# Performance work log

Hardware: AMD Instinct MI355X
Metric: run time of the kernel (lower is better)

## Reference

```python
import jax, jax.numpy as jnp
import numpy as np

N, E, H = 20000, 320000, 5
IND, OUT = 64, 64
D2 = 2 * OUT          # 128
CAT = OUT + D2        # 192
BN_EPS = 1e-5


def _bn(x, g, b, m, v):
    # eval-mode BatchNorm1d
    return (x - m) * jax.lax.rsqrt(v + BN_EPS) * g + b


def _gcn(x, W, b, src, dst, n):
    # PyG GCNConv: add self-loops (already in src/dst), sym-normalized aggregation
    h = x @ W                                             # [N, C]
    deg = jax.ops.segment_sum(jnp.ones_like(dst, dtype=h.dtype), dst, num_segments=n)
    dinv = jnp.where(deg > 0, jax.lax.rsqrt(deg), 0.0)
    norm = dinv[src] * dinv[dst]                          # [E']
    out = jax.ops.segment_sum(h[src] * norm[:, None], dst, num_segments=n)
    return out + b


def _gat(x, W, att_src, att_dst, b, src, dst, n, heads, c):
    # PyG GATConv (concat=False): per-edge attention, segment softmax over dst
    hx = (x @ W).reshape(n, heads, c)                     # [N, H, C]
    a_s = jnp.einsum('nhc,hc->nh', hx, att_src)           # [N, H]
    a_d = jnp.einsum('nhc,hc->nh', hx, att_dst)
    e = jax.nn.leaky_relu(a_s[src] + a_d[dst], 0.2)       # [E', H]
    m = jax.ops.segment_max(e, dst, num_segments=n)       # every node has a self-loop
    w = jnp.exp(e - m[dst])
    den = jax.ops.segment_sum(w, dst, num_segments=n)
    alpha = w / den[dst]                                  # [E', H]
    out = jax.ops.segment_sum(hx[src] * alpha[:, :, None], dst, num_segments=n)  # [N,H,C]
    return out.mean(axis=1) + b


def setup_inputs() -> dict:
    key = jax.random.key(0)
    ks = iter(jax.random.split(key, 64))
    rn = lambda *s: jax.random.normal(next(ks), s, dtype=jnp.float32) * 0.05
    d = {}
    d['x_in'] = jax.random.normal(next(ks), (N, IND), dtype=jnp.float32)
    d['edge_index'] = jax.random.randint(next(ks), (2, E), 0, N, dtype=jnp.int64)
    # nn1: indim -> 2*indim -> outdim -> 2*outdim
    d['nn1_w1'], d['nn1_b1'] = rn(IND, 2 * IND), rn(2 * IND)
    d['nn1_w2'], d['nn1_b2'] = rn(2 * IND, OUT), rn(OUT)
    d['nn1_w3'], d['nn1_b3'] = rn(OUT, D2), rn(D2)
    # batchnorms (eval mode: gamma, beta, running mean/var)
    for name, dim in (('bn0', D2), ('bn1', D2), ('bn2', OUT)):
        d[name + '_g'] = rn(dim) + 1.0
        d[name + '_b'] = rn(dim)
        d[name + '_m'] = rn(dim)
        d[name + '_v'] = jax.random.uniform(next(ks), (dim,), jnp.float32, 0.5, 1.5)
    d['gcn1_w'], d['gcn1_b'] = rn(D2, D2), rn(D2)
    d['gat1_w'] = rn(D2, H * D2)
    d['gat1_as'], d['gat1_ad'], d['gat1_b'] = rn(H, D2), rn(H, D2), rn(D2)
    d['gcn2_w'], d['gcn2_b'] = rn(D2, OUT), rn(OUT)
    d['gat2_w'] = rn(OUT, H * OUT)
    d['gat2_as'], d['gat2_ad'], d['gat2_b'] = rn(H, OUT), rn(H, OUT), rn(OUT)
    # node_pred MLP: 192 -> 96 -> 48 -> 24 -> 1
    d['mlp_w1'], d['mlp_b1'] = rn(CAT, CAT // 2), rn(CAT // 2)
    d['mlp_w2'], d['mlp_b2'] = rn(CAT // 2, CAT // 4), rn(CAT // 4)
    d['mlp_w3'], d['mlp_b3'] = rn(CAT // 4, CAT // 8), rn(CAT // 8)
    d['mlp_w4'], d['mlp_b4'] = rn(CAT // 8, 1), rn(1)
    return d


def reference(x_in, edge_index,
              nn1_w1, nn1_b1, nn1_w2, nn1_b2, nn1_w3, nn1_b3,
              bn0_g, bn0_b, bn0_m, bn0_v,
              gcn1_w, gcn1_b, gat1_w, gat1_as, gat1_ad, gat1_b,
              gcn2_w, gcn2_b, gat2_w, gat2_as, gat2_ad, gat2_b,
              bn1_g, bn1_b, bn1_m, bn1_v,
              bn2_g, bn2_b, bn2_m, bn2_v,
              mlp_w1, mlp_b1, mlp_w2, mlp_b2, mlp_w3, mlp_b3, mlp_w4, mlp_b4):
    n = x_in.shape[0]
    loop = jnp.arange(n, dtype=edge_index.dtype)
    src = jnp.concatenate([edge_index[0], loop])   # self-loops (GCN & GAT defaults)
    dst = jnp.concatenate([edge_index[1], loop])

    sp = jax.nn.softplus
    x = sp(x_in @ nn1_w1 + nn1_b1)
    x = sp(x @ nn1_w2 + nn1_b2)
    x = x @ nn1_w3 + nn1_b3
    x = jax.nn.leaky_relu(_bn(x, bn0_g, bn0_b, bn0_m, bn0_v), 0.01)

    x1 = _gcn(x, gcn1_w, gcn1_b, src, dst, n)
    x1 = _gat(x1, gat1_w, gat1_as, gat1_ad, gat1_b, src, dst, n, H, D2)
    x1 = jax.nn.leaky_relu(_bn(x1, bn1_g, bn1_b, bn1_m, bn1_v), 0.01)
    skip1 = x + x1

    x2 = _gcn(skip1, gcn2_w, gcn2_b, src, dst, n)
    x2 = _gat(x2, gat2_w, gat2_as, gat2_ad, gat2_b, src, dst, n, H, OUT)
    x2 = jax.nn.leaky_relu(_bn(x2, bn2_g, bn2_b, bn2_m, bn2_v), 0.01)

    xf = jnp.concatenate([skip1, x2], axis=1)      # [N, 192]
    h = sp(xf @ mlp_w1 + mlp_b1)
    h = sp(h @ mlp_w2 + mlp_b2)
    h = sp(h @ mlp_w3 + mlp_b3)
    node_probs = jax.nn.sigmoid(h @ mlp_w4 + mlp_b4)   # [N, 1]
    return xf, node_probs
```

## Files before the change

kernel.cpp:

```cpp
#include <hip/hip_runtime.h>
#include <hip/hip_bf16.h>
#include <math.h>
#include <stdint.h>

typedef __hip_bfloat16 bf16;
typedef __hip_bfloat162 bf162;
typedef __attribute__((ext_vector_type(8))) short short8;
typedef __attribute__((ext_vector_type(4))) float f32x4;
#define HEADS 5

static inline long long cdivll(long long a, long long b){ return (a + b - 1) / b; }

__device__ __forceinline__ float b2f(bf16 v){ return __bfloat162float(v); }
__device__ __forceinline__ bf16 f2b(float v){ return __float2bfloat16(v); }
__device__ __forceinline__ short f2bs(float x){ bf16 b = __float2bfloat16(x); return *reinterpret_cast<short*>(&b); }
__device__ __forceinline__ float ldp(const void* p, long long i, int f32){
  return f32 ? ((const float*)p)[i] : b2f(((const bf16*)p)[i]);
}
__device__ __forceinline__ int eidx(const int* ei, long long i, int i64){
  return i64 ? ei[2 * i] : ei[i];
}
__device__ __forceinline__ float lrelu(float x, float a){ return x >= 0.f ? x : a * x; }
__device__ __forceinline__ float splus(float x){ return fmaxf(x, 0.f) + log1pf(expf(-fabsf(x))); }

__global__ void k_detect(const unsigned short* xh, const int* ei, int* flags){
  __shared__ int r0[256], r1[256];
  int t = threadIdx.x;
  int nan_cnt = 0;
  for (int i = t; i < 8192; i += 256){
    unsigned short u = xh[i];
    if (((u >> 7) & 0xFF) == 0xFF) nan_cnt++;
  }
  int odd_nz = 0;
  for (int i = 1 + 2 * t; i < 1024; i += 512) if (ei[i] != 0) odd_nz++;
  r0[t] = nan_cnt; r1[t] = odd_nz; __syncthreads();
  for (int o = 128; o > 0; o >>= 1){
    if (t < o){ r0[t] += r0[t + o]; r1[t] += r1[t + o]; }
    __syncthreads();
  }
  if (t == 0){
    flags[0] = (r0[0] > 0) ? 1 : 0;
    flags[1] = (r1[0] == 0) ? 1 : 0;
  }
}

__global__ void k_stampfill(bf16* out, long long n, float code){
  long long i = (long long)blockIdx.x * blockDim.x + threadIdx.x;
  if (i < n) out[i] = f2b(i == 0 ? code : 0.f);
}

__global__ void k_hist(const int* ei, int E, int N, int* counts, const int* flags){
  int i64 = flags[1];
  int e = blockIdx.x * blockDim.x + threadIdx.x;
  if (e >= E + N) return;
  int d = (e < E) ? eidx(ei, (long long)E + e, i64) : (e - E);
  atomicAdd(&counts[d], 1);
}
__global__ __launch_bounds__(1024) void k_scan(const int* counts, int* rowptr, int N){
  __shared__ int sums[1024];
  int t = threadIdx.x;
  int chunk = (N + 1023) / 1024;
  int start = t * chunk;
  int end = start + chunk; if (end > N) end = N;
  int s = 0;
  for (int i = start; i < end; ++i) s += counts[i];
  sums[t] = s; __syncthreads();
  for (int o = 1; o < 1024; o <<= 1){
    int v = (t >= o) ? sums[t - o] : 0;
    __syncthreads();
    sums[t] += v;
    __syncthreads();
  }
  int run = (t == 0) ? 0 : sums[t - 1];
  for (int i = start; i < end; ++i){ rowptr[i] = run; run += counts[i]; }
  if (t == 0) rowptr[N] = sums[1023];
}
__global__ void k_scatter(const int* ei, int E, int N, const int* rowptr, int* cursor,
                          unsigned short* colu, const int* flags){
  int i64 = flags[1];
  int e = blockIdx.x * blockDim.x + threadIdx.x;
  if (e >= E + N) return;
  int s, d;
  if (e < E){ s = eidx(ei, e, i64); d = eidx(ei, (long long)E + e, i64); }
  else { s = d = e - E; }
  int pos = rowptr[d] + atomicAdd(&cursor[d], 1);
  colu[pos] = (unsigned short)s;
}
__global__ void k_dinv(const int* rowptr, float* dinv, int N){
  int i = blockIdx.x * blockDim.x + threadIdx.x;
  if (i < N) dinv[i] = rsqrtf((float)(rowptr[i + 1] - rowptr[i]));
}

struct PackDesc { const void* W; int K, Kp, C, Cp, off, hk; };
struct PackArgs { PackDesc d[10]; int total; };
__global__ void k_packall(PackArgs P, bf16* WTA, int* cnt, int ncnt, const int* flags){
  int f32 = flags[0];
  int idx = blockIdx.x * blockDim.x + threadIdx.x;
  if (idx >= P.total){
    int z = idx - P.total;
    if (z < ncnt) cnt[z] = 0;
    return;
  }
  int base = 0;
#pragma unroll
  for (int s = 0; s < 10; ++s){
    int sz = P.d[s].Kp * P.d[s].Cp;
    if (idx < base + sz){
      int local = idx - base;
      int c = local / P.d[s].Kp;
      int k = local - c * P.d[s].Kp;
      float v;
      if (P.d[s].hk){
        int h = k / P.d[s].K;
        int kk = k - h * P.d[s].K;
        v = (c < P.d[s].C)
          ? ldp(P.d[s].W, (long long)kk * (P.d[s].hk * P.d[s].C) + h * P.d[s].C + c, f32) : 0.f;
      } else {
        v = (k < P.d[s].K && c < P.d[s].C)
          ? ldp(P.d[s].W, (long long)k * P.d[s].C + c, f32) : 0.f;
      }
      WTA[P.d[s].off + local] = f2b(v);
      return;
    }
    base += sz;
  }
}

__global__ void k_att_fold(const void* w1, const void* as1, const void* ad1,
                           const void* w2, const void* as2, const void* ad2,
                           bf16* wta, const int* flags){
  int f32 = flags[0];
  int idx = blockIdx.x * blockDim.x + threadIdx.x;
  if (idx < 8192){
    int c = idx >> 7, k = idx & 127;
    float v = 0.f;
    if (c < 10){
      int h = (c < 5) ? c : c - 5;
      const void* aw = (c < 5) ? as1 : ad1;
      for (int j = 0; j < 128; ++j)
        v = fmaf(ldp(w1, (long long)k * 640 + h * 128 + j, f32), ldp(aw, h * 128 + j, f32), v);
    }
    wta[186368 + idx] = f2b(v);
  } else if (idx < 12288){
    int l = idx - 8192;
    int c = l >> 6, k = l & 63;
    float v = 0.f;
    if (c < 10){
      int h = (c < 5) ? c : c - 5;
      const void* aw = (c < 5) ? as2 : ad2;
      for (int j = 0; j < 64; ++j)
        v = fmaf(ldp(w2, (long long)k * 320 + h * 64 + j, f32), ldp(aw, h * 64 + j, f32), v);
    }
    wta[194560 + l] = f2b(v);
  }
}

__global__ __launch_bounds__(256) void k_proj128(
    const void* in, int ik, int ldin, const bf16* WT, bf16* outb,
    int N, int Cp, const int* flags)
{
  __shared__ float red[2][16][68];
  int f32 = flags[0];
  int use_b16 = (ik == 2 && !f32);
  int t = threadIdx.x;
  int wave = t >> 6, lane = t & 63;
  int quad = lane >> 4, l15 = lane & 15;
  int rowgrp = wave & 1, kh = wave >> 1;
  int mbase = blockIdx.x * 32 + rowgrp * 16;
  int c0 = blockIdx.y * 64;
  f32x4 acc[4];
#pragma unroll
  for (int j = 0; j < 4; ++j) acc[j] = (f32x4){0.f, 0.f, 0.f, 0.f};

  int m = mbase + l15; if (m > N - 1) m = N - 1;

#pragma unroll
  for (int ki = 0; ki < 2; ++ki){
    int ka = kh * 64 + ki * 32 + quad * 8;
    short8 af;
    if (use_b16){
      af = *(const short8*)((const bf16*)in + (size_t)m * ldin + ka);
    } else {
      const float* p = (const float*)in + (size_t)m * ldin + ka;
      float4 v0 = *(const float4*)p;
      float4 v1 = *(const float4*)(p + 4);
      af[0] = f2bs(v0.x); af[1] = f2bs(v0.y); af[2] = f2bs(v0.z); af[3] = f2bs(v0.w);
      af[4] = f2bs(v1.x); af[5] = f2bs(v1.y); af[6] = f2bs(v1.z); af[7] = f2bs(v1.w);
    }
#pragma unroll
    for (int j = 0; j < 4; ++j){
      short8 bvv = *(const short8*)(WT + (size_t)(c0 + 16 * j + l15) * 128 + ka);
      acc[j] = __builtin_amdgcn_mfma_f32_16x16x32_bf16(af, bvv, acc[j], 0, 0, 0);
    }
  }

  if (kh == 1){
#pragma unroll
    for (int j = 0; j < 4; ++j)
#pragma unroll
      for (int r = 0; r < 4; ++r)
        red[rowgrp][quad * 4 + r][16 * j + l15] = acc[j][r];
  }
  __syncthreads();
  if (kh == 1) return;
#pragma unroll
  for (int j = 0; j < 4; ++j)
#pragma unroll
    for (int r = 0; r < 4; ++r)
      acc[j][r] += red[rowgrp][quad * 4 + r][16 * j + l15];

#pragma unroll
  for (int j = 0; j < 4; ++j){
    int c = c0 + 16 * j + l15;
#pragma unroll
    for (int r = 0; r < 4; ++r){
      int n = mbase + quad * 4 + r;
      if (n < N) outb[(size_t)n * Cp + c] = f2b(acc[j][r]);
    }
  }
}

__global__ __launch_bounds__(256) void k_nn1f(
    const void* xin, const bf16* WTA,
    const void* b1, const void* b2, const void* b3,
    const void* g0, const void* bb0, const void* m0, const void* v0,
    float* X, int N, const int* flags)
{
  __shared__ bf16 s1[4][16][136];
  __shared__ bf16 s2[4][16][72];
  int f32 = flags[0];
  int t = threadIdx.x, wave = t >> 6, lane = t & 63;
  int quad = lane >> 4, l15 = lane & 15;
  int mbase = blockIdx.x * 64 + wave * 16;
  int m = mbase + l15; if (m > N - 1) m = N - 1;

  f32x4 a1[8];
#pragma unroll
  for (int j = 0; j < 8; ++j) a1[j] = (f32x4){0.f, 0.f, 0.f, 0.f};
#pragma unroll
  for (int k0 = 0; k0 < 64; k0 += 32){
    int ka = k0 + quad * 8;
    short8 af;
    if (!f32){
      af = *(const short8*)((const bf16*)xin + (size_t)m * 64 + ka);
    } else {
      const float* p = (const float*)xin + (size_t)m * 64 + ka;
      float4 v0 = *(const float4*)p;
      float4 v1 = *(const float4*)(p + 4);
      af[0] = f2bs(v0.x); af[1] = f2bs(v0.y); af[2] = f2bs(v0.z); af[3] = f2bs(v0.w);
      af[4] = f2bs(v1.x); af[5] = f2bs(v1.y); af[6] = f2bs(v1.z); af[7] = f2bs(v1.w);
    }
#pragma unroll
    for (int j = 0; j < 8; ++j){
      short8 bvv = *(const short8*)(WTA + (size_t)(16 * j + l15) * 64 + ka);
      a1[j] = __builtin_amdgcn_mfma_f32_16x16x32_bf16(af, bvv, a1[j], 0, 0, 0);
    }
  }
#pragma unroll
  for (int j = 0; j < 8; ++j){
    int c = 16 * j + l15;
    float bi = ldp(b1, c, f32);
#pragma unroll
    for (int r = 0; r < 4; ++r)
      s1[wave][quad * 4 + r][c] = f2b(splus(a1[j][r] + bi));
  }
  __syncthreads();

  f32x4 a2[4];
#pragma unroll
  for (int j = 0; j < 4; ++j) a2[j] = (f32x4){0.f, 0.f, 0.f, 0.f};
#pragma unroll
  for (int k0 = 0; k0 < 128; k0 += 32){
    int ka = k0 + quad * 8;
    short8 af = *(const short8*)&s1[wave][l15][ka];
#pragma unroll
    for (int j = 0; j < 4; ++j){
      short8 bvv = *(const short8*)(WTA + 8192 + (size_t)(16 * j + l15) * 128 + ka);
      a2[j] = __builtin_amdgcn_mfma_f32_16x16x32_bf16(af, bvv, a2[j], 0, 0, 0);
    }
  }
#pragma unroll
  for (int j = 0; j < 4; ++j){
    int c = 16 * j + l15;
    float bi = ldp(b2, c, f32);
#pragma unroll
    for (int r = 0; r < 4; ++r)
      s2[wave][quad * 4 + r][c] = f2b(splus(a2[j][r] + bi));
  }
  __syncthreads();

  f32x4 a3[8];
#pragma unroll
  for (int j = 0; j < 8; ++j) a3[j] = (f32x4){0.f, 0.f, 0.f, 0.f};
#pragma unroll
  for (int k0 = 0; k0 < 64; k0 += 32){
    int ka = k0 + quad * 8;
    short8 af = *(const short8*)&s2[wave][l15][ka];
#pragma unroll
    for (int j = 0; j < 8; ++j){
      short8 bvv = *(const short8*)(WTA + 16384 + (size_t)(16 * j + l15) * 64 + ka);
      a3[j] = __builtin_amdgcn_mfma_f32_16x16x32_bf16(af, bvv, a3[j], 0, 0, 0);
    }
  }
#pragma unroll
  for (int j = 0; j < 8; ++j){
    int c = 16 * j + l15;
    float bi = ldp(b3, c, f32);
    float g = ldp(g0, c, f32), be = ldp(bb0, c, f32), mm = ldp(m0, c, f32);
    float iv = rsqrtf(ldp(v0, c, f32) + 1e-5f);
#pragma unroll
    for (int r = 0; r < 4; ++r){
      int n = mbase + quad * 4 + r;
      if (n >= N) continue;
      float y = a3[j][r] + bi;
      y = (y - mm) * iv * g + be;
      X[(size_t)n * 128 + c] = lrelu(y, 0.01f);
    }
  }
}

__global__ __launch_bounds__(256) void k_mlpf(
    const void* dout, const bf16* WTA,
    const void* b1, const void* b2, const void* b3,
    const void* w4, const void* b4, void* outfin, int N, const int* flags)
{
  __shared__ bf16 s1[4][16][104];
  __shared__ bf16 s2[4][16][72];
  int f32 = flags[0];
  int t = threadIdx.x, wave = t >> 6, lane = t & 63;
  int quad = lane >> 4, l15 = lane & 15;
  int mbase = blockIdx.x * 64 + wave * 16;
  int m = mbase + l15; if (m > N - 1) m = N - 1;

  f32x4 a1[6];
#pragma unroll
  for (int j = 0; j < 6; ++j) a1[j] = (f32x4){0.f, 0.f, 0.f, 0.f};
#pragma unroll
  for (int k0 = 0; k0 < 192; k0 += 32){
    int ka = k0 + quad * 8;
    short8 af;
    if (!f32){
      af = *(const short8*)((const bf16*)dout + (size_t)m * 192 + ka);
    } else {
      const float* p = (const float*)dout + (size_t)m * 192 + ka;
      float4 v0 = *(const float4*)p;
      float4 v1 = *(const float4*)(p + 4);
      af[0] = f2bs(v0.x); af[1] = f2bs(v0.y); af[2] = f2bs(v0.z); af[3] = f2bs(v0.w);
      af[4] = f2bs(v1.x); af[5] = f2bs(v1.y); af[6] = f2bs(v1.z); af[7] = f2bs(v1.w);
    }
#pragma unroll
    for (int j = 0; j < 6; ++j){
      short8 bvv = *(const short8*)(WTA + 151552 + (size_t)(16 * j + l15) * 192 + ka);
      a1[j] = __builtin_amdgcn_mfma_f32_16x16x32_bf16(af, bvv, a1[j], 0, 0, 0);
    }
  }
#pragma unroll
  for (int j = 0; j < 6; ++j){
    int c = 16 * j + l15;
    float bi = ldp(b1, c, f32);
#pragma unroll
    for (int r = 0; r < 4; ++r)
      s1[wave][quad * 4 + r][c] = f2b(splus(a1[j][r] + bi));
  }
  __syncthreads();

  f32x4 a2[3];
#pragma unroll
  for (int j = 0; j < 3; ++j) a2[j] = (f32x4){0.f, 0.f, 0.f, 0.f};
#pragma unroll
  for (int k0 = 0; k0 < 96; k0 += 32){
    int ka = k0 + quad * 8;
    short8 af = *(const short8*)&s1[wave][l15][ka];
#pragma unroll
    for (int j = 0; j < 3; ++j){
      short8 bvv = *(const short8*)(WTA + 176128 + (size_t)(16 * j + l15) * 96 + ka);
      a2[j] = __builtin_amdgcn_mfma_f32_16x16x32_bf16(af, bvv, a2[j], 0, 0, 0);
    }
  }
#pragma unroll
  for (int j = 0; j < 4; ++j){
    int c = 16 * j + l15;
    if (j < 3){
      float bi = ldp(b2, c, f32);
#pragma unroll
      for (int r = 0; r < 4; ++r)
        s2[wave][quad * 4 + r][c] = f2b(splus(a2[j][r] + bi));
    } else {
#pragma unroll
      for (int r = 0; r < 4; ++r)
        s2[wave][quad * 4 + r][c] = f2b(0.f);
    }
  }
  __syncthreads();

  f32x4 a3[2];
#pragma unroll
  for (int j = 0; j < 2; ++j) a3[j] = (f32x4){0.f, 0.f, 0.f, 0.f};
#pragma unroll
  for (int k0 = 0; k0 < 64; k0 += 32){
    int ka = k0 + quad * 8;
    short8 af = *(const short8*)&s2[wave][l15][ka];
#pragma unroll
    for (int j = 0; j < 2; ++j){
      short8 bvv = *(const short8*)(WTA + 182272 + (size_t)(16 * j + l15) * 64 + ka);
      a3[j] = __builtin_amdgcn_mfma_f32_16x16x32_bf16(af, bvv, a3[j], 0, 0, 0);
    }
  }
  float pr[4] = {0.f, 0.f, 0.f, 0.f};
#pragma unroll
  for (int j = 0; j < 2; ++j){
    int c = 16 * j + l15;
    float w = (c < 24) ? ldp(w4, c, f32) : 0.f;
    float bi = (c < 24) ? ldp(b3, c, f32) : 0.f;
#pragma unroll
    for (int r = 0; r < 4; ++r)
      pr[r] = fmaf(splus(a3[j][r] + bi), w, pr[r]);
  }
#pragma unroll
  for (int r = 0; r < 4; ++r){
#pragma unroll
    for (int o = 1; o < 16; o <<= 1) pr[r] += __shfl_xor(pr[r], o);
    int n = mbase + quad * 4 + r;
    if (l15 == 0 && n < N){
      float p = 1.f / (1.f + expf(-(pr[r] + ldp(b4, 0, f32))));
      long long oi = (long long)N * 192 + n;
      if (f32) ((float*)outfin)[oi] = p; else ((bf16*)outfin)[oi] = f2b(p);
    }
  }
}

__global__ __launch_bounds__(256) void k_gcn_csr(
    const int* rowptr, const unsigned short* colu, const bf16* h,
    const float* dinv, const void* bias, bf16* outb, int N, int C,
    const bf16* watt, float* asd, const int* flags)
{
  int f32 = flags[0];
  int wid = (blockIdx.x * 256 + threadIdx.x) >> 6;
  int lane = threadIdx.x & 63;
  if (wid >= N) return;
  int i0 = rowptr[wid], i1 = rowptr[wid + 1];
  float dr = dinv[wid];
  if (C == 128){
    int coff = lane << 1;
    float ax[4] = {0.f, 0.f, 0.f, 0.f}, ay[4] = {0.f, 0.f, 0.f, 0.f};
    int i = i0;
    for (; i + 3 < i1; i += 4){
      int s[4] = {colu[i], colu[i + 1], colu[i + 2], colu[i + 3]};
#pragma unroll
      for (int e = 0; e < 4; ++e){
        bf162 v = *(const bf162*)(h + (size_t)s[e] * 128 + coff);
        float f = dinv[s[e]];
        ax[e] = fmaf(f, b2f(v.x), ax[e]); ay[e] = fmaf(f, b2f(v.y), ay[e]);
      }
    }
    for (; i < i1; ++i){
      int s0 = colu[i];
      bf162 v = *(const bf162*)(h + (size_t)s0 * 128 + coff);
      float f = dinv[s0];
      ax[0] = fmaf(f, b2f(v.x), ax[0]); ay[0] = fmaf(f, b2f(v.y), ay[0]);
    }
    float sx = (ax[0] + ax[1]) + (ax[2] + ax[3]);
    float sy = (ay[0] + ay[1]) + (ay[2] + ay[3]);
    float vx = sx * dr + ldp(bias, coff, f32);
    float vy = sy * dr + ldp(bias, coff + 1, f32);
    bf162 o; o.x = f2b(vx); o.y = f2b(vy);
    *(bf162*)(outb + (size_t)wid * 128 + coff) = o;
    if (watt){
      float myv = 0.f;
#pragma unroll
      for (int hh = 0; hh < 10; ++hh){
        bf162 w = *(const bf162*)(watt + hh * 128 + coff);
        float p = vx * b2f(w.x) + vy * b2f(w.y);
#pragma unroll
        for (int o2 = 1; o2 < 64; o2 <<= 1) p += __shfl_xor(p, o2);
        if (lane == hh) myv = p;
      }
      if (lane < 10) asd[(size_t)wid * 10 + lane] = myv;
    }
  } else {
    int half = lane >> 5, hl = lane & 31;
    int coff = hl << 1;
    float ax = 0.f, ay = 0.f, bx = 0.f, by = 0.f;
    int i = i0;
    for (; i + 3 < i1; i += 4){
      int sA = colu[i + half], sB = colu[i + 2 + half];
      bf162 vA = *(const bf162*)(h + (size_t)sA * 64 + coff);
      bf162 vB = *(const bf162*)(h + (size_t)sB * 64 + coff);
      float fA = dinv[sA], fB = dinv[sB];
      ax = fmaf(fA, b2f(vA.x), ax); ay = fmaf(fA, b2f(vA.y), ay);
      bx = fmaf(fB, b2f(vB.x), bx); by = fmaf(fB, b2f(vB.y), by);
    }
    for (; i + 1 < i1; i += 2){
      int s = colu[i + half];
      bf162 v = *(const bf162*)(h + (size_t)s * 64 + coff);
      float f = dinv[s];
      ax = fmaf(f, b2f(v.x), ax); ay = fmaf(f, b2f(v.y), ay);
    }
    if (i < i1 && half == 0){
      int s = colu[i];
      bf162 v = *(const bf162*)(h + (size_t)s * 64 + coff);
      float f = dinv[s];
      ax = fmaf(f, b2f(v.x), ax); ay = fmaf(f, b2f(v.y), ay);
    }
    ax += bx; ay += by;
    ax += __shfl_xor(ax, 32);
    ay += __shfl_xor(ay, 32);
    float vx = ax * dr + ldp(bias, coff, f32);
    float vy = ay * dr + ldp(bias, coff + 1, f32);
    if (half == 0){
      bf162 o; o.x = f2b(vx); o.y = f2b(vy);
      *(bf162*)(outb + (size_t)wid * 64 + coff) = o;
    }
    if (watt){
      float myv = 0.f;
#pragma unroll
      for (int hh = 0; hh < 10; ++hh){
        bf162 w = *(const bf162*)(watt + hh * 64 + coff);
        float p = vx * b2f(w.x) + vy * b2f(w.y);
#pragma unroll
        for (int o2 = 1; o2 < 32; o2 <<= 1) p += __shfl_xor(p, o2);
        if (lane == hh) myv = p;
      }
      if (lane < 10) asd[(size_t)wid * 10 + lane] = myv;
    }
  }
}

template<int K>
__global__ __launch_bounds__(256) void k_gat_proj(
    const int* rowptr, const unsigned short* colu, const bf16* bbx,
    const float* asd, const bf16* WT, const void* bias,
    const void* bg, const void* bbp, const void* bm, const void* bv,
    const float* skip, void* dout, int c2off, int N, const int* flags)
{
  constexpr int KP  = HEADS * K;
  constexpr int AGP = (K == 128) ? 648 : 328;
  constexpr int C   = K;
  constexpr int NJ  = C / 64;
  __shared__ bf16 agg[16][AGP];
  __shared__ float als[4][HEADS][64];
  __shared__ unsigned short ssrc[4][64];
  int f32 = flags[0];
  int t = threadIdx.x, wave = t >> 6, lane = t & 63;
  int quad = lane >> 4, l15 = lane & 15;
  int rb = blockIdx.x * 16;

  for (int q = 0; q < 4; ++q){
    int lr = wave * 4 + q;
    int wid = rb + lr;
    if (wid >= N) break;
    int i0 = rowptr[wid], i1 = rowptr[wid + 1];
    float adr[HEADS];
#pragma unroll
    for (int h = 0; h < HEADS; ++h) adr[h] = asd[(size_t)wid * 10 + 5 + h];
    float mx[HEADS];
#pragma unroll
    for (int h = 0; h < HEADS; ++h) mx[h] = -1e30f;
    for (int i = i0 + lane; i < i1; i += 64){
      int s = colu[i];
#pragma unroll
      for (int h = 0; h < HEADS; ++h){
        float e = lrelu(asd[(size_t)s * 10 + h] + adr[h], 0.2f);
        mx[h] = fmaxf(mx[h], e);
      }
    }
#pragma unroll
    for (int h = 0; h < HEADS; ++h)
      for (int o = 32; o > 0; o >>= 1) mx[h] = fmaxf(mx[h], __shfl_xor(mx[h], o));
    float den[HEADS];
#pragma unroll
    for (int h = 0; h < HEADS; ++h) den[h] = 0.f;
    for (int i = i0 + lane; i < i1; i += 64){
      int s = colu[i];
#pragma unroll
      for (int h = 0; h < HEADS; ++h){
        float e = lrelu(asd[(size_t)s * 10 + h] + adr[h], 0.2f);
        den[h] += expf(e - mx[h]);
      }
    }
#pragma unroll
    for (int h = 0; h < HEADS; ++h){
      for (int o = 32; o > 0; o >>= 1) den[h] += __shfl_xor(den[h], o);
      den[h] = 1.f / (den[h] * (float)HEADS);
    }
    if constexpr (K == 128){
      int coff = lane << 1;
      float ax[HEADS], ay[HEADS];
#pragma unroll
      for (int h = 0; h < HEADS; ++h){ ax[h] = 0.f; ay[h] = 0.f; }
      for (int base = i0; base < i1; base += 64){
        int iend = i1 - base; if (iend > 64) iend = 64;
        int i = base + lane;
        if (i < i1){
          int s = colu[i];
          ssrc[wave][lane] = (unsigned short)s;
#pragma unroll
          for (int h = 0; h < HEADS; ++h){
            float e = lrelu(asd[(size_t)s * 10 + h] + adr[h], 0.2f);
            als[wave][h][lane] = expf(e - mx[h]) * den[h];
          }
        }
        asm volatile("s_waitcnt lgkmcnt(0)" ::: "memory");
        int j = 0;
        for (; j + 3 < iend; j += 4){
          int s4[4];
#pragma unroll
          for (int e = 0; e < 4; ++e) s4[e] = ssrc[wave][j + e];
          bf162 v[4];
#pragma unroll
          for (int e = 0; e < 4; ++e) v[e] = *(const bf162*)(bbx + (size_t)s4[e] * 128 + coff);
#pragma unroll
          for (int e = 0; e < 4; ++e){
            float fx = b2f(v[e].x), fy = b2f(v[e].y);
#pragma unroll
            for (int h = 0; h < HEADS; ++h){
              float a = als[wave][h][j + e];
              ax[h] = fmaf(a, fx, ax[h]); ay[h] = fmaf(a, fy, ay[h]);
            }
          }
        }
        for (; j < iend; ++j){
          int s = ssrc[wave][j];
          bf162 v = *(const bf162*)(bbx + (size_t)s * 128 + coff);
          float fx = b2f(v.x), fy = b2f(v.y);
#pragma unroll
          for (int h = 0; h < HEADS; ++h){
            float a = als[wave][h][j];
            ax[h] = fmaf(a, fx, ax[h]); ay[h] = fmaf(a, fy, ay[h]);
          }
        }
      }
#pragma unroll
      for (int h = 0; h < HEADS; ++h){
        bf162 o; o.x = f2b(ax[h]); o.y = f2b(ay[h]);
        *(bf162*)&agg[lr][h * 128 + coff] = o;
      }
    } else {
      int half = lane >> 5, hl = lane & 31;
      int coff = hl << 1;
      float ax[HEADS], ay[HEADS];
#pragma unroll
      for (int h = 0; h < HEADS; ++h){ ax[h] = 0.f; ay[h] = 0.f; }
      for (int base = i0; base < i1; base += 64){
        int iend = i1 - base; if (iend > 64) iend = 64;
        int i = base + lane;
        if (i < i1){
          int s = colu[i];
          ssrc[wave][lane] = (unsigned short)s;
#pragma unroll
          for (int h = 0; h < HEADS; ++h){
            float e = lrelu(asd[(size_t)s * 10 + h] + adr[h], 0.2f);
            als[wave][h][lane] = expf(e - mx[h]) * den[h];
          }
        }
        asm volatile("s_waitcnt lgkmcnt(0)" ::: "memory");
        int j = 0;
        for (; j + 3 < iend; j += 4){
          int sA = ssrc[wave][j + half], sB = ssrc[wave][j + 2 + half];
          bf162 vA = *(const bf162*)(bbx + (size_t)sA * 64 + coff);
          bf162 vB = *(const bf162*)(bbx + (size_t)sB * 64 + coff);
          float Ax = b2f(vA.x), Ay = b2f(vA.y), Bx = b2f(vB.x), By = b2f(vB.y);
#pragma unroll
          for (int h = 0; h < HEADS; ++h){
            float aA = als[wave][h][j + half], aB = als[wave][h][j + 2 + half];
            ax[h] = fmaf(aA, Ax, ax[h]); ay[h] = fmaf(aA, Ay, ay[h]);
            ax[h] = fmaf(aB, Bx, ax[h]); ay[h] = fmaf(aB, By, ay[h]);
          }
        }
        for (; j + 1 < iend; j += 2){
          int s = ssrc[wave][j + half];
          bf162 v = *(const bf162*)(bbx + (size_t)s * 64 + coff);
          float fx = b2f(v.x), fy = b2f(v.y);
#pragma unroll
          for (int h = 0; h < HEADS; ++h){
            float a = als[wave][h][j + half];
            ax[h] = fmaf(a, fx, ax[h]); ay[h] = fmaf(a, fy, ay[h]);
          }
        }
        if (j < iend && half == 0){
          int s = ssrc[wave][j];
          bf162 v = *(const bf162*)(bbx + (size_t)s * 64 + coff);
          float fx = b2f(v.x), fy = b2f(v.y);
#pragma unroll
          for (int h = 0; h < HEADS; ++h){
            float a = als[wave][h][j];
            ax[h] = fmaf(a, fx, ax[h]); ay[h] = fmaf(a, fy, ay[h]);
          }
        }
      }
#pragma unroll
      for (int h = 0; h < HEADS; ++h){
        ax[h] += __shfl_xor(ax[h], 32);
        ay[h] += __shfl_xor(ay[h], 32);
      }
      if (half == 0){
#pragma unroll
        for (int h = 0; h < HEADS; ++h){
          bf162 o; o.x = f2b(ax[h]); o.y = f2b(ay[h]);
          *(bf162*)&agg[lr][h * 64 + coff] = o;
        }
      }
    }
  }
  __syncthreads();

  f32x4 acc[NJ];
#pragma unroll
  for (int j = 0; j < NJ; ++j) acc[j] = (f32x4){0.f, 0.f, 0.f, 0.f};
  int c0 = wave * (16 * NJ);
#pragma unroll
  for (int k0 = 0; k0 < KP; k0 += 32){
    int ka = k0 + quad * 8;
    short8 af = *(const short8*)&agg[l15][ka];
#pragma unroll
    for (int j = 0; j < NJ; ++j){
      short8 bvv = *(const short8*)(WT + (size_t)(c0 + 16 * j + l15) * KP + ka);
      acc[j] = __builtin_amdgcn_mfma_f32_16x16x32_bf16(af, bvv, acc[j], 0, 0, 0);
    }
  }
#pragma unroll
  for (int j = 0; j < NJ; ++j){
    int c = c0 + 16 * j + l15;
    float bi = ldp(bias, c, f32);
    float g = ldp(bg, c, f32), be = ldp(bbp, c, f32), mm = ldp(bm, c, f32);
    float iv = rsqrtf(ldp(bv, c, f32) + 1e-5f);
#pragma unroll
    for (int r = 0; r < 4; ++r){
      int n = rb + quad * 4 + r;
      if (n >= N) continue;
      float y = acc[j][r] + bi;
      y = (y - mm) * iv * g + be;
      y = lrelu(y, 0.01f);
      if (skip) y += skip[(size_t)n * 128 + c];
      size_t o = (size_t)n * 192 + c2off + c;
      if (f32) ((float*)dout)[o] = y; else ((bf16*)dout)[o] = f2b(y);
    }
  }
}

extern "C" void kernel_launch(void* const* d_in, const int* in_sizes, int n_in,
                              void* d_out, int out_size, void* d_ws, size_t ws_size,
                              hipStream_t stream)
{
  const void* x_in   = d_in[0];
  const int*  ei     = (const int*)d_in[1];
  const void *nn1_w1 = d_in[2], *nn1_b1 = d_in[3], *nn1_w2 = d_in[4], *nn1_b2 = d_in[5];
  const void *nn1_w3 = d_in[6], *nn1_b3 = d_in[7];
  const void *bn0_g = d_in[8],  *bn0_b = d_in[9],  *bn0_m = d_in[10], *bn0_v = d_in[11];
  const void *bn1_g = d_in[12], *bn1_b = d_in[13], *bn1_m = d_in[14], *bn1_v = d_in[15];
  const void *bn2_g = d_in[16], *bn2_b = d_in[17], *bn2_m = d_in[18], *bn2_v = d_in[19];
  const void *gcn1_w = d_in[20], *gcn1_b = d_in[21];
  const void *gat1_w = d_in[22], *gat1_as = d_in[23], *gat1_ad = d_in[24], *gat1_b = d_in[25];
  const void *gcn2_w = d_in[26], *gcn2_b = d_in[27];
  const void *gat2_w = d_in[28], *gat2_as = d_in[29], *gat2_ad = d_in[30], *gat2_b = d_in[31];
  const void *mlp_w1 = d_in[32], *mlp_b1 = d_in[33], *mlp_w2 = d_in[34], *mlp_b2 = d_in[35];
  const void *mlp_w3 = d_in[36], *mlp_b3 = d_in[37], *mlp_w4 = d_in[38], *mlp_b4 = d_in[39];
  (void)n_in;

  const int N  = in_sizes[0] / 64;
  const int E  = in_sizes[1] / 2;
  const int Ep = E + N;
  const int TB = 256;

  if ((long long)out_size != (long long)N * 193 || N > 65535){
    k_stampfill<<<(int)cdivll(out_size, TB), TB, 0, stream>>>((bf16*)d_out, out_size, 8192.f);
    return;
  }
  size_t need = 2900ull * (size_t)N + 500000ull;
  if (ws_size < need){
    k_stampfill<<<(int)cdivll(out_size, TB), TB, 0, stream>>>((bf16*)d_out, out_size, 1024.f);
    return;
  }

  char* wsb = (char*)d_ws;
  int*   FLAGS = (int*)wsb;
  float* X    = (float*)(wsb + 16);
  float* A    = X + (size_t)N * 128;
  float* B    = A + (size_t)N * 128;
  float* DINV = B + (size_t)N * 128;
  float* AS   = DINV + N;
  int*   ROWP = (int*)(AS + (size_t)N * 2 * HEADS);
  unsigned short* COLU = (unsigned short*)(ROWP + N + 1);
  bf16*  HX   = (bf16*)(COLU + ((Ep + 7) & ~7));
  bf16*  WTA  = (bf16*)(((uintptr_t)(HX + (size_t)N * 640) + 15) & ~(uintptr_t)15);
  bf16*  BB   = (bf16*)A;
  int* CNT = (int*)AS;
  int* CUR = CNT + N;
  const int ATT1_OFF = 186368;
  const int ATT2_OFF = 194560;

  k_detect<<<1, 256, 0, stream>>>((const unsigned short*)x_in, ei, FLAGS);

  PackArgs P;
  P.d[0] = {nn1_w1,  64, 64, 128, 128, 0, 0};
  P.d[1] = {nn1_w2, 128,128,  64,  64, 8192, 0};
  P.d[2] = {nn1_w3,  64, 64, 128, 128, 16384, 0};
  P.d[3] = {gcn1_w, 128,128, 128, 128, 24576, 0};
  P.d[4] = {gat1_w, 128,640, 128, 128, 40960, 5};
  P.d[5] = {gcn2_w, 128,128,  64,  64, 122880, 0};
  P.d[6] = {gat2_w,  64,320,  64,  64, 131072, 5};
  P.d[7] = {mlp_w1, 192,192,  96, 128, 151552, 0};
  P.d[8] = {mlp_w2,  96, 96,  48,  64, 176128, 0};
  P.d[9] = {mlp_w3,  48, 64,  24,  64, 182272, 0};
  P.total = 186368;
  k_packall<<<(int)cdivll(P.total + 2 * N, TB), TB, 0, stream>>>(P, WTA, CNT, 2 * N, FLAGS);
  k_att_fold<<<48, 256, 0, stream>>>(gat1_w, gat1_as, gat1_ad, gat2_w, gat2_as, gat2_ad, WTA, FLAGS);

  k_hist<<<(int)cdivll(Ep, TB), TB, 0, stream>>>(ei, E, N, CNT, FLAGS);
  k_scan<<<1, 1024, 0, stream>>>(CNT, ROWP, N);
  k_scatter<<<(int)cdivll(Ep, TB), TB, 0, stream>>>(ei, E, N, ROWP, CUR, COLU, FLAGS);
  k_dinv<<<(int)cdivll(N, TB), TB, 0, stream>>>(ROWP, DINV, N);

  int rowsg = (int)cdivll(N, 4);
  int rowsf = (int)cdivll(N, 64);
  int rows16 = (int)cdivll(N, 16);

  k_nn1f<<<rowsf, 256, 0, stream>>>(x_in, WTA, nn1_b1, nn1_b2, nn1_b3,
                                    bn0_g, bn0_b, bn0_m, bn0_v, X, N, FLAGS);

  k_proj128<<<dim3((unsigned)cdivll(N, 32), 2), 256, 0, stream>>>(
      X, 0, 128, WTA + 24576, HX, N, 128, FLAGS);
  k_gcn_csr<<<rowsg, 256, 0, stream>>>(ROWP, COLU, HX, DINV, gcn1_b, BB, N, 128,
                                       WTA + ATT1_OFF, AS, FLAGS);

  k_gat_proj<128><<<rows16, 256, 0, stream>>>(ROWP, COLU, BB, AS, WTA + 40960, gat1_b,
      bn1_g, bn1_b, bn1_m, bn1_v, X, d_out, 0, N, FLAGS);

  k_proj128<<<dim3((unsigned)cdivll(N, 32), 1), 256, 0, stream>>>(
      d_out, 2, 192, WTA + 122880, HX, N, 64, FLAGS);
  k_gcn_csr<<<rowsg, 256, 0, stream>>>(ROWP, COLU, HX, DINV, gcn2_b, BB, N, 64,
                                       WTA + ATT2_OFF, AS, FLAGS);

  k_gat_proj<64><<<rows16, 256, 0, stream>>>(ROWP, COLU, BB, AS, WTA + 131072, gat2_b,
      bn2_g, bn2_b, bn2_m, bn2_v, nullptr, d_out, 128, N, FLAGS);

  k_mlpf<<<rowsf, 256, 0, stream>>>(d_out, WTA, mlp_b1, mlp_b2, mlp_b3,
                                    mlp_w4, mlp_b4, d_out, N, FLAGS);
}
```

Baseline: 468.8 us.

## Use one wave per node in GAT projection kernel with split-K MFMA reduction

The fused GAT aggregation and projection kernel now launches 1024 threads per block, so each of 16 waves aggregates one destination node instead of 4 waves looping over 4 nodes each. The projection GEMM is reorganized so each wave computes one 16-column group over half of the K dimension. The two halves are summed through shared memory reused from the attention buffer. This raises parallelism for the latency-bound edge gather, at the cost of larger blocks, more shared memory and an extra barrier. For K=64, half of the waves sit idle during the GEMM.

Result: no change. 461.6 us (-1.5%).

```diff
diff --git a/kernel.cpp b/kernel.cpp
--- a/kernel.cpp
+++ b/kernel.cpp
@@ -527,7 +527,7 @@
 }
 
 template<int K>
-__global__ __launch_bounds__(256) void k_gat_proj(
+__global__ __launch_bounds__(1024) void k_gat_proj(
     const int* rowptr, const unsigned short* colu, const bf16* bbx,
     const float* asd, const bf16* WT, const void* bias,
     const void* bg, const void* bbp, const void* bm, const void* bv,
@@ -536,19 +536,18 @@
   constexpr int KP  = HEADS * K;
   constexpr int AGP = (K == 128) ? 648 : 328;
   constexpr int C   = K;
-  constexpr int NJ  = C / 64;
+  constexpr int NCG = C / 16;
+  constexpr int KSEG = KP / 2;
   __shared__ bf16 agg[16][AGP];
-  __shared__ float als[4][HEADS][64];
-  __shared__ unsigned short ssrc[4][64];
+  __shared__ float als[16][HEADS][64];
+  __shared__ unsigned short ssrc[16][64];
   int f32 = flags[0];
   int t = threadIdx.x, wave = t >> 6, lane = t & 63;
   int quad = lane >> 4, l15 = lane & 15;
   int rb = blockIdx.x * 16;
 
-  for (int q = 0; q < 4; ++q){
-    int lr = wave * 4 + q;
-    int wid = rb + lr;
-    if (wid >= N) break;
+  int wid = rb + wave;
+  if (wid < N){
     int i0 = rowptr[wid], i1 = rowptr[wid + 1];
     float adr[HEADS];
 #pragma unroll
@@ -633,7 +632,7 @@
 #pragma unroll
       for (int h = 0; h < HEADS; ++h){
         bf162 o; o.x = f2b(ax[h]); o.y = f2b(ay[h]);
-        *(bf162*)&agg[lr][h * 128 + coff] = o;
+        *(bf162*)&agg[wave][h * 128 + coff] = o;
       }
     } else {
       int half = lane >> 5, hl = lane & 31;
@@ -697,44 +696,51 @@
 #pragma unroll
         for (int h = 0; h < HEADS; ++h){
           bf162 o; o.x = f2b(ax[h]); o.y = f2b(ay[h]);
-          *(bf162*)&agg[lr][h * 64 + coff] = o;
+          *(bf162*)&agg[wave][h * 64 + coff] = o;
         }
       }
     }
   }
   __syncthreads();
 
-  f32x4 acc[NJ];
-#pragma unroll
-  for (int j = 0; j < NJ; ++j) acc[j] = (f32x4){0.f, 0.f, 0.f, 0.f};
-  int c0 = wave * (16 * NJ);
-#pragma unroll
-  for (int k0 = 0; k0 < KP; k0 += 32){
-    int ka = k0 + quad * 8;
-    short8 af = *(const short8*)&agg[l15][ka];
-#pragma unroll
-    for (int j = 0; j < NJ; ++j){
-      short8 bvv = *(const short8*)(WT + (size_t)(c0 + 16 * j + l15) * KP + ka);
-      acc[j] = __builtin_amdgcn_mfma_f32_16x16x32_bf16(af, bvv, acc[j], 0, 0, 0);
-    }
-  }
-#pragma unroll
-  for (int j = 0; j < NJ; ++j){
-    int c = c0 + 16 * j + l15;
-    float bi = ldp(bias, c, f32);
-    float g = ldp(bg, c, f32), be = ldp(bbp, c, f32), mm = ldp(bm, c, f32);
-    float iv = rsqrtf(ldp(bv, c, f32) + 1e-5f);
-#pragma unroll
-    for (int r = 0; r < 4; ++r){
-      int n = rb + quad * 4 + r;
-      if (n >= N) continue;
-      float y = acc[j][r] + bi;
-      y = (y - mm) * iv * g + be;
-      y = lrelu(y, 0.01f);
-      if (skip) y += skip[(size_t)n * 128 + c];
-      size_t o = (size_t)n * 192 + c2off + c;
-      if (f32) ((float*)dout)[o] = y; else ((bf16*)dout)[o] = f2b(y);
-    }
+  auto red = reinterpret_cast<float(*)[16][17]>(&als[0][0][0]);
+  int cg = wave & (NCG - 1);
+  int kh = wave / NCG;
+  f32x4 acc = (f32x4){0.f, 0.f, 0.f, 0.f};
+  if (kh < 2){
+#pragma unroll
+    for (int ks = 0; ks < KSEG; ks += 32){
+      int ka = kh * KSEG + ks + quad * 8;
+      short8 af = *(const short8*)&agg[l15][ka];
+      short8 bvv = *(const short8*)(WT + (size_t)(cg * 16 + l15) * KP + ka);
+      acc = __builtin_amdgcn_mfma_f32_16x16x32_bf16(af, bvv, acc, 0, 0, 0);
+    }
+  }
+  if (kh == 1){
+#pragma unroll
+    for (int r = 0; r < 4; ++r)
+      red[cg][quad * 4 + r][l15] = acc[r];
+  }
+  __syncthreads();
+  if (kh != 0) return;
+#pragma unroll
+  for (int r = 0; r < 4; ++r)
+    acc[r] += red[cg][quad * 4 + r][l15];
+
+  int c = cg * 16 + l15;
+  float bi = ldp(bias, c, f32);
+  float g = ldp(bg, c, f32), be = ldp(bbp, c, f32), mm = ldp(bm, c, f32);
+  float iv = rsqrtf(ldp(bv, c, f32) + 1e-5f);
+#pragma unroll
+  for (int r = 0; r < 4; ++r){
+    int n = rb + quad * 4 + r;
+    if (n >= N) continue;
+    float y = acc[r] + bi;
+    y = (y - mm) * iv * g + be;
+    y = lrelu(y, 0.01f);
+    if (skip) y += skip[(size_t)n * 128 + c];
+    size_t o = (size_t)n * 192 + c2off + c;
+    if (f32) ((float*)dout)[o] = y; else ((bf16*)dout)[o] = f2b(y);
   }
 }
 
@@ -823,7 +829,7 @@
   k_gcn_csr<<<rowsg, 256, 0, stream>>>(ROWP, COLU, HX, DINV, gcn1_b, BB, N, 128,
                                        WTA + ATT1_OFF, AS, FLAGS);
 
-  k_gat_proj<128><<<rows16, 256, 0, stream>>>(ROWP, COLU, BB, AS, WTA + 40960, gat1_b,
+  k_gat_proj<128><<<rows16, 1024, 0, stream>>>(ROWP, COLU, BB, AS, WTA + 40960, gat1_b,
       bn1_g, bn1_b, bn1_m, bn1_v, X, d_out, 0, N, FLAGS);
 
   k_proj128<<<dim3((unsigned)cdivll(N, 32), 1), 256, 0, stream>>>(
@@ -831,7 +837,7 @@
   k_gcn_csr<<<rowsg, 256, 0, stream>>>(ROWP, COLU, HX, DINV, gcn2_b, BB, N, 64,
                                        WTA + ATT2_OFF, AS, FLAGS);
 
-  k_gat_proj<64><<<rows16, 256, 0, stream>>>(ROWP, COLU, BB, AS, WTA + 131072, gat2_b,
+  k_gat_proj<64><<<rows16, 1024, 0, stream>>>(ROWP, COLU, BB, AS, WTA + 131072, gat2_b,
       bn2_g, bn2_b, bn2_m, bn2_v, nullptr, d_out, 128, N, FLAGS);
 
   k_mlpf<<<rowsf, 256, 0, stream>>>(d_out, WTA, mlp_b1, mlp_b2, mlp_b3,
```
